# Kernel tuning notes

Hardware: AMD Instinct MI355X
Metric: run time of the kernel (lower is better)

The kernel has to match this reference:

```python
import jax, jax.numpy as jnp
import numpy as np

NH, NUM_H, NUM_W = 8, 4, 4  # num_heads, patch_size


def _grid_sample_zeros(img, grid):
    # img: (N, C, H, W); grid: (N, Ho, Wo, 2) with grid[...,0]=x, grid[...,1]=y in [-1,1]
    # bilinear, align_corners=True, padding_mode='zeros' (each out-of-range tap contributes 0)
    N, C, H, W = img.shape
    gx = (grid[..., 0] + 1.0) * 0.5 * (W - 1)
    gy = (grid[..., 1] + 1.0) * 0.5 * (H - 1)
    x0 = jnp.floor(gx)
    y0 = jnp.floor(gy)
    x1 = x0 + 1.0
    y1 = y0 + 1.0
    wx1 = gx - x0
    wx0 = 1.0 - wx1
    wy1 = gy - y0
    wy0 = 1.0 - wy1

    def per_n(img_n, x0n, x1n, y0n, y1n, w00, w01, w10, w11):
        def tap(xi, yi, w):
            valid = (xi >= 0) & (xi <= W - 1) & (yi >= 0) & (yi <= H - 1)
            xc = jnp.clip(xi, 0, W - 1).astype(jnp.int32)
            yc = jnp.clip(yi, 0, H - 1).astype(jnp.int32)
            return img_n[:, yc, xc] * (w * valid)[None]  # (C, Ho, Wo)
        return tap(x0n, y0n, w00) + tap(x1n, y0n, w01) + tap(x0n, y1n, w10) + tap(x1n, y1n, w11)

    return jax.vmap(per_n)(img, x0, x1, y0, y1, wx0 * wy0, wx1 * wy0, wx0 * wy1, wx1 * wy1)


def _forward(x, global_center, fd_w, fd_b, off_w, off_b, scale_w, scale_b,
             angle_w, angle_b, q_w, q_b, k_w, k_b, v_w, v_b, proj_w, proj_b,
             conv1_w, bn1_g, bn1_b, bn1_m, bn1_v, conv2_w, bn2_g, bn2_b, bn2_m, bn2_v):
    B, C, H, W = x.shape
    K = fd_w.shape[0]
    nh, num_h, num_w = NH, NUM_H, NUM_W
    hd = C // nh
    ws_h, ws_w = H // num_h, W // num_w
    nW = num_h * num_w
    npt = B * nh  # num_predict_total (num_deform = 1)
    S = ws_h * ws_w
    leaky = lambda z: jnp.where(z > 0, z, 0.01 * z)

    # class probabilities: 1x1 conv + softmax over all spatial positions
    logits = jnp.einsum('bchw,kc->bkhw', x, fd_w) + fd_b[None, :, None, None]
    probs = jax.nn.softmax(logits.reshape(B, K, H * W), axis=-1).reshape(B, K, H, W)

    # per-window adaptive-avg-pooled features -> offsets / scales / angles (1x1 convs)
    pooled = leaky(x.reshape(B, C, num_h, ws_h, num_w, ws_w).mean(axis=(3, 5)))  # (B,C,num_h,num_w)

    def head_conv(wt, bi, last):
        o = jnp.einsum('bcij,oc->boij', pooled, wt) + bi[None, :, None, None]
        o = o.transpose(0, 2, 3, 1).reshape(B, num_h, num_w, nh, last)
        return o.transpose(0, 3, 4, 1, 2).reshape(B * nh, last, num_h, num_w)

    off = head_conv(off_w, off_b, 2)
    off = off / jnp.array([H // num_h, W // num_w], jnp.float32)[None, :, None, None]
    scl = head_conv(scale_w, scale_b, 2)
    ang = head_conv(angle_w, angle_b, 1)

    # reference / base coordinates (channel 0 = x/width coord, channel 1 = y/height coord)
    h_lin = jnp.linspace(-1.0, 1.0, H)
    w_lin = jnp.linspace(-1.0, 1.0, W)
    wr_h = h_lin.reshape(num_h, ws_h).mean(axis=1)  # window centers (avg_pool)
    wr_w = w_lin.reshape(num_w, ws_w).mean(axis=1)
    bh = jnp.arange(ws_h, dtype=jnp.float32) * 2.0 / (H - 1)
    bh = bh - bh.mean()
    bw = jnp.arange(ws_w, dtype=jnp.float32) * 2.0 / (W - 1)
    bw = bw - bw.mean()

    # scaled then rotated window coords + offsets; shapes broadcast to (npt,num_h,ws_h,num_w,ws_w)
    wc0 = bw[None, None, None, None, :] * (scl[:, 0, :, None, :, None] + 1.0)
    wc1 = bh[None, None, :, None, None] * (scl[:, 1, :, None, :, None] + 1.0)
    a = ang[:, 0, :, None, :, None]
    sin_a, cos_a = jnp.sin(a), jnp.cos(a)
    r0 = -wc1 * sin_a + wc0 * cos_a
    r1 = wc1 * cos_a + wc0 * sin_a
    c0 = wr_w[None, None, None, :, None] + r0 + off[:, 0, :, None, :, None]
    c1 = wr_h[None, :, None, None, None] + r1 + off[:, 1, :, None, :, None]
    grid = jnp.stack([c0, c1], axis=-1).reshape(npt, H, W, 2)

    # keys over the full map, reshaped so each head-block is sampled by its own grid
    key_feat = jnp.einsum('bhwc,oc->bhwo', x.transpose(0, 2, 3, 1), k_w) + k_b
    key_feat = key_feat.transpose(0, 3, 1, 2).reshape(npt, hd, H, W)
    tx = _grid_sample_zeros(key_feat, grid)
    tx = tx.reshape(npt, hd, num_h, ws_h, num_w, ws_w).transpose(0, 2, 4, 3, 5, 1).reshape(npt * nW, S, hd)

    # probs tiled with torch .repeat semantics (index i -> batch i % B), then sampled
    tp = _grid_sample_zeros(jnp.tile(probs, (nh, 1, 1, 1)), grid)
    tp = tp.reshape(npt, K, num_h, ws_h, num_w, ws_w).transpose(0, 2, 4, 3, 5, 1).reshape(npt * nW, S, K)

    # local class centers; reshape matches torch's raw view (B*nW, nh, K, hd)
    lc = jnp.einsum('nsk,nsd->nkd', tp, tx).reshape(B * nW, nh, K, hd)

    # windowed queries, values from global centers (torch .repeat tiling semantics)
    xw = x.reshape(B, C, num_h, ws_h, num_w, ws_w).transpose(0, 2, 4, 3, 5, 1).reshape(B * nW, S, C)
    q = (xw @ q_w.T + q_b).reshape(B * nW, S, nh, hd).transpose(0, 2, 1, 3)  # (BnW, nh, S, hd)
    gc_rep = jnp.tile(global_center, (nW, 1, 1))
    v = (gc_rep @ v_w.T + v_b).reshape(B * nW, K, nh, hd).transpose(0, 2, 1, 3)  # (BnW, nh, K, hd)

    scale = float(hd) ** -0.5
    dots = jnp.einsum('bnsd,bnkd->bnsk', q, lc) * scale
    attn = jax.nn.softmax(dots, axis=-1)
    out = jnp.einsum('bnsk,bnkd->bnsd', attn, v)  # (BnW, nh, S, hd)

    ctx = out.transpose(0, 2, 1, 3).reshape(B * nW, S, C)
    ctx = (ctx @ proj_w.T + proj_b).transpose(0, 2, 1).reshape(B * nW, C, ws_h, ws_w)
    # patch_recover -> (B, C, H, W)
    ctx = ctx.reshape(B, num_h, num_w, C, ws_h, ws_w).transpose(0, 3, 1, 4, 2, 5).reshape(B, C, H, W)

    def conv_bn_relu(h, wconv, g, bb, m, var):
        h = jax.lax.conv_general_dilated(h, wconv, (1, 1), 'SAME',
                                         dimension_numbers=('NCHW', 'OIHW', 'NCHW'))
        h = (h - m[None, :, None, None]) * jax.lax.rsqrt(var + 1e-5)[None, :, None, None]
        h = h * g[None, :, None, None] + bb[None, :, None, None]
        return jnp.maximum(h, 0.0)

    h1 = jnp.concatenate([x, ctx], axis=1)  # (B, 2C, H, W)
    h1 = conv_bn_relu(h1, conv1_w, bn1_g, bn1_b, bn1_m, bn1_v)
    h1 = conv_bn_relu(h1, conv2_w, bn2_g, bn2_b, bn2_m, bn2_v)  # Dropout2d = identity (eval)
    return h1


def setup_inputs():
    B, C, H, W, K, nh = 2, 512, 128, 128, 32, NH
    ks = jax.random.split(jax.random.key(0), 16)

    def lin(k, o, i, s=1.0):
        return (jax.random.normal(k, (o, i), jnp.float32) * (s / np.sqrt(i))).astype(jnp.float32)

    return {
        'x': jax.random.normal(ks[0], (B, C, H, W), jnp.float32),
        'global_center': jax.random.normal(ks[1], (B, K, C), jnp.float32),
        'fd_w': lin(ks[2], K, C), 'fd_b': jnp.zeros((K,), jnp.float32),
        'off_w': lin(ks[3], nh * 2, C, 4.0), 'off_b': jnp.zeros((nh * 2,), jnp.float32),
        'scale_w': lin(ks[4], nh * 2, C, 4.0), 'scale_b': jnp.zeros((nh * 2,), jnp.float32),
        'angle_w': lin(ks[5], nh, C, 4.0), 'angle_b': jnp.zeros((nh,), jnp.float32),
        'q_w': lin(ks[6], C, C), 'q_b': jnp.zeros((C,), jnp.float32),
        'k_w': lin(ks[7], C, C), 'k_b': jnp.zeros((C,), jnp.float32),
        'v_w': lin(ks[8], C, C), 'v_b': jnp.zeros((C,), jnp.float32),
        'proj_w': lin(ks[9], C, C), 'proj_b': jnp.zeros((C,), jnp.float32),
        'conv1_w': jax.random.normal(ks[10], (C, 2 * C, 3, 3), jnp.float32) / np.sqrt(2 * C * 9.0),
        'bn1_g': jnp.ones((C,), jnp.float32), 'bn1_b': jnp.zeros((C,), jnp.float32),
        'bn1_m': jnp.zeros((C,), jnp.float32), 'bn1_v': jnp.ones((C,), jnp.float32),
        'conv2_w': jax.random.normal(ks[11], (C, C, 3, 3), jnp.float32) / np.sqrt(C * 9.0),
        'bn2_g': jnp.ones((C,), jnp.float32), 'bn2_b': jnp.zeros((C,), jnp.float32),
        'bn2_m': jnp.zeros((C,), jnp.float32), 'bn2_v': jnp.ones((C,), jnp.float32),
    }


def reference(x, global_center, fd_w, fd_b, off_w, off_b, scale_w, scale_b,
              angle_w, angle_b, q_w, q_b, k_w, k_b, v_w, v_b, proj_w, proj_b,
              conv1_w, bn1_g, bn1_b, bn1_m, bn1_v, conv2_w, bn2_g, bn2_b, bn2_m, bn2_v):
    return _forward(x, global_center, fd_w, fd_b, off_w, off_b, scale_w, scale_b,
                    angle_w, angle_b, q_w, q_b, k_w, k_b, v_w, v_b, proj_w, proj_b,
                    conv1_w, bn1_g, bn1_b, bn1_m, bn1_v, conv2_w, bn2_g, bn2_b, bn2_m, bn2_v)
```

## Files before the change

### kernel.cpp

```cpp
#include <hip/hip_runtime.h>
#include <hip/hip_bf16.h>
#include <math.h>

#define HW 16384
#define IMH 128
#define IMW 128

typedef _Float16 f16x8 __attribute__((ext_vector_type(8)));
typedef float f32x4 __attribute__((ext_vector_type(4)));

__device__ __forceinline__ void gload16(const void* g, void* l) {
  __builtin_amdgcn_global_load_lds(
      (const __attribute__((address_space(1))) void*)g,
      (__attribute__((address_space(3))) void*)l, 16, 0, 0);
}

__global__ __launch_bounds__(256) void k_logits(const float* __restrict__ x,
                                                const float* __restrict__ fd_w,
                                                const float* __restrict__ fd_b,
                                                float* __restrict__ probs) {
  __shared__ float w[256 * 32];
  int b = blockIdx.y;
  int pix = blockIdx.x * 256 + threadIdx.x;
  float acc[32];
#pragma unroll
  for (int k = 0; k < 32; k++) acc[k] = fd_b[k];
  const float* xp = x + (size_t)b * 512 * HW + pix;
  for (int half = 0; half < 2; half++) {
    int cbase = half * 256;
    __syncthreads();
    for (int i = threadIdx.x; i < 256 * 32; i += 256) {
      int c = i >> 5, k = i & 31;
      w[i] = fd_w[k * 512 + cbase + c];
    }
    __syncthreads();
    for (int c = 0; c < 256; c++) {
      float xv = xp[(size_t)(cbase + c) * HW];
#pragma unroll
      for (int k = 0; k < 32; k++) acc[k] += xv * w[c * 32 + k];
    }
  }
#pragma unroll
  for (int k = 0; k < 32; k++) probs[((size_t)(b * 32 + k)) * HW + pix] = acc[k];
}

__global__ __launch_bounds__(256) void k_softmax_sp(float* __restrict__ probs) {
  int row = blockIdx.x;
  float* p = probs + (size_t)row * HW;
  __shared__ float red[256];
  float mx = -1e30f;
  for (int i = threadIdx.x; i < HW; i += 256) mx = fmaxf(mx, p[i]);
  red[threadIdx.x] = mx;
  __syncthreads();
  for (int s = 128; s > 0; s >>= 1) {
    if (threadIdx.x < s) red[threadIdx.x] = fmaxf(red[threadIdx.x], red[threadIdx.x + s]);
    __syncthreads();
  }
  mx = red[0];
  __syncthreads();
  float sum = 0.f;
  for (int i = threadIdx.x; i < HW; i += 256) sum += expf(p[i] - mx);
  red[threadIdx.x] = sum;
  __syncthreads();
  for (int s = 128; s > 0; s >>= 1) {
    if (threadIdx.x < s) red[threadIdx.x] += red[threadIdx.x + s];
    __syncthreads();
  }
  float inv = 1.0f / red[0];
  for (int i = threadIdx.x; i < HW; i += 256) p[i] = expf(p[i] - mx) * inv;
}

__global__ __launch_bounds__(256) void k_pool(const float* __restrict__ x,
                                              float* __restrict__ pooled) {
  int b = blockIdx.z, ih = blockIdx.y, iw = blockIdx.x;
  for (int c = threadIdx.x; c < 512; c += 256) {
    const float* xp = x + ((size_t)(b * 512 + c) * IMH + ih * 32) * IMW + iw * 32;
    float s = 0.f;
    for (int r = 0; r < 32; r++)
      for (int cc = 0; cc < 32; cc++) s += xp[r * IMW + cc];
    s *= (1.0f / 1024.0f);
    if (s < 0.f) s *= 0.01f;
    pooled[(b * 512 + c) * 16 + ih * 4 + iw] = s;
  }
}

__global__ __launch_bounds__(256) void k_heads(const float* __restrict__ pooled,
                                               const float* __restrict__ off_w, const float* __restrict__ off_b,
                                               const float* __restrict__ scale_w, const float* __restrict__ scale_b,
                                               const float* __restrict__ angle_w, const float* __restrict__ angle_b,
                                               float* __restrict__ f_off, float* __restrict__ f_scl,
                                               float* __restrict__ f_ang) {
  int b = blockIdx.z, ih = blockIdx.y, iw = blockIdx.x;
  __shared__ float pl[512];
  int ij = ih * 4 + iw;
  for (int c = threadIdx.x; c < 512; c += 256) pl[c] = pooled[(b * 512 + c) * 16 + ij];
  __syncthreads();
  int t = threadIdx.x;
  if (t < 40) {
    const float* wt;
    float bias;
    if (t < 16) { wt = off_w + t * 512; bias = off_b[t]; }
    else if (t < 32) { int u = t - 16; wt = scale_w + u * 512; bias = scale_b[u]; }
    else { int u = t - 32; wt = angle_w + u * 512; bias = angle_b[u]; }
    float s = bias;
    for (int c = 0; c < 512; c++) s += pl[c] * wt[c];
    if (t < 16) {
      int n = t / 2, l = t % 2;
      f_off[((b * 8 + n) * 2 + l) * 16 + ij] = s * (1.0f / 32.0f);
    } else if (t < 32) {
      int u = t - 16;
      int n = u / 2, l = u % 2;
      f_scl[((b * 8 + n) * 2 + l) * 16 + ij] = s;
    } else {
      int n = t - 32;
      f_ang[(b * 8 + n) * 16 + ij] = s;
    }
  }
}

__global__ __launch_bounds__(256) void k_grid(const float* __restrict__ f_off,
                                              const float* __restrict__ f_scl,
                                              const float* __restrict__ f_ang,
                                              float* __restrict__ grid) {
  int p = blockIdx.y;
  int hw = blockIdx.x * 256 + threadIdx.x;
  int h = hw >> 7, w = hw & 127;
  int ih = h >> 5, r = h & 31, iw = w >> 5, cs = w & 31;
  int ij = ih * 4 + iw;
  float off0 = f_off[(p * 2 + 0) * 16 + ij], off1 = f_off[(p * 2 + 1) * 16 + ij];
  float scl0 = f_scl[(p * 2 + 0) * 16 + ij], scl1 = f_scl[(p * 2 + 1) * 16 + ij];
  float a = f_ang[p * 16 + ij];
  float sa = sinf(a), ca = cosf(a);
  float bwv = ((float)cs - 15.5f) * (2.0f / 127.0f);
  float bhv = ((float)r - 15.5f) * (2.0f / 127.0f);
  float wc0 = bwv * (scl0 + 1.0f);
  float wc1 = bhv * (scl1 + 1.0f);
  float wrw = -1.0f + 2.0f * ((float)(iw * 32) + 15.5f) / 127.0f;
  float wrh = -1.0f + 2.0f * ((float)(ih * 32) + 15.5f) / 127.0f;
  float c0 = wrw + (-wc1 * sa + wc0 * ca) + off0;
  float c1 = wrh + (wc1 * ca + wc0 * sa) + off1;
  size_t o = ((size_t)p * HW + hw) * 2;
  grid[o] = c0;
  grid[o + 1] = c1;
}

__global__ __launch_bounds__(256) void k_gsample(const float* __restrict__ img, int CH, int pmod,
                                                 const float* __restrict__ grid,
                                                 float* __restrict__ out) {
  int p = blockIdx.y;
  int hw = blockIdx.x * 256 + threadIdx.x;
  const float* ib = img + (size_t)(p % pmod) * CH * HW;
  float gx = grid[((size_t)p * HW + hw) * 2 + 0];
  float gy = grid[((size_t)p * HW + hw) * 2 + 1];
  gx = (gx + 1.0f) * 0.5f * 127.0f;
  gy = (gy + 1.0f) * 0.5f * 127.0f;
  float x0f = floorf(gx), y0f = floorf(gy);
  float wx1 = gx - x0f, wx0 = 1.0f - wx1;
  float wy1 = gy - y0f, wy0 = 1.0f - wy1;
  int x0 = (int)x0f, y0 = (int)y0f;
  bool vx0 = (x0f >= 0.f) && (x0f <= 127.f);
  bool vx1 = (x0f + 1.0f >= 0.f) && (x0f + 1.0f <= 127.f);
  bool vy0 = (y0f >= 0.f) && (y0f <= 127.f);
  bool vy1 = (y0f + 1.0f >= 0.f) && (y0f + 1.0f <= 127.f);
  int x0c = min(max(x0, 0), 127), x1c = min(max(x0 + 1, 0), 127);
  int y0c = min(max(y0, 0), 127), y1c = min(max(y0 + 1, 0), 127);
  float w00 = wx0 * wy0 * ((vx0 && vy0) ? 1.f : 0.f);
  float w01 = wx1 * wy0 * ((vx1 && vy0) ? 1.f : 0.f);
  float w10 = wx0 * wy1 * ((vx0 && vy1) ? 1.f : 0.f);
  float w11 = wx1 * wy1 * ((vx1 && vy1) ? 1.f : 0.f);
  int o00 = y0c * IMW + x0c, o01 = y0c * IMW + x1c;
  int o10 = y1c * IMW + x0c, o11 = y1c * IMW + x1c;
  for (int c = 0; c < CH; c++) {
    const float* ic = ib + (size_t)c * HW;
    float v = ic[o00] * w00 + ic[o01] * w01 + ic[o10] * w10 + ic[o11] * w11;
    out[((size_t)p * CH + c) * HW + hw] = v;
  }
}

__global__ __launch_bounds__(256) void k_lc(const float* __restrict__ tx,
                                            const float* __restrict__ tp,
                                            float* __restrict__ lc) {
  int idx2 = blockIdx.x;
  int p = idx2 >> 4, win = idx2 & 15;
  int ih = win >> 2, iw = win & 3;
  __shared__ float ltx[64][65];
  __shared__ float ltp[64][33];
  int tid = threadIdx.x;
  int k = tid >> 3, dg = tid & 7;
  float acc[8] = {};
  const float* txp = tx + (size_t)p * 64 * HW;
  const float* tpp = tp + (size_t)p * 32 * HW;
  int base = (ih * 32) * IMW + iw * 32;
  for (int s0 = 0; s0 < 1024; s0 += 64) {
#pragma unroll
    for (int i = 0; i < 16; i++) {
      int linear = tid + i * 256;
      int d = linear >> 6, sl = linear & 63;
      int s = s0 + sl;
      int pix = base + (s >> 5) * IMW + (s & 31);
      ltx[sl][d] = txp[(size_t)d * HW + pix];
    }
#pragma unroll
    for (int i = 0; i < 8; i++) {
      int linear = tid + i * 256;
      int kk = linear >> 6, sl = linear & 63;
      int s = s0 + sl;
      int pix = base + (s >> 5) * IMW + (s & 31);
      ltp[sl][kk] = tpp[(size_t)kk * HW + pix];
    }
    __syncthreads();
    for (int sl = 0; sl < 64; sl++) {
      float tv = ltp[sl][k];
#pragma unroll
      for (int j = 0; j < 8; j++) acc[j] += tv * ltx[sl][dg * 8 + j];
    }
    __syncthreads();
  }
  float* lp = lc + ((size_t)idx2 * 32 + k) * 64 + dg * 8;
#pragma unroll
  for (int j = 0; j < 8; j++) lp[j] = acc[j];
}

__global__ __launch_bounds__(256) void k_v2(const float* __restrict__ gc,
                                            const float* __restrict__ v_w,
                                            const float* __restrict__ v_b,
                                            float* __restrict__ v2) {
  int j = blockIdx.x >> 5, k = blockIdx.x & 31;
  __shared__ float g[512];
  for (int c = threadIdx.x; c < 512; c += 256) g[c] = gc[((size_t)j * 32 + k) * 512 + c];
  __syncthreads();
  for (int o = threadIdx.x; o < 512; o += 256) {
    float s = v_b[o];
    const float* wp = v_w + (size_t)o * 512;
    for (int c = 0; c < 512; c++) s += g[c] * wp[c];
    v2[((size_t)j * 32 + k) * 512 + o] = s;
  }
}

__global__ __launch_bounds__(256) void k_attn(const float* __restrict__ Yq,
                                              const float* __restrict__ lc,
                                              const float* __restrict__ v2,
                                              _Float16* __restrict__ att) {
  int n = blockIdx.x, win = blockIdx.y, b = blockIdx.z;
  int ih = win >> 2, iw = win & 3;
  __shared__ float llc[32 * 64];
  __shared__ float lv[32 * 64];
  int bnw = b * 16 + win;
  const float* lcp = lc + (size_t)(bnw * 8 + n) * 2048;
  const float* vp = v2 + (size_t)(bnw & 1) * 32 * 512 + n * 64;
  for (int i = threadIdx.x; i < 2048; i += 256) {
    llc[i] = lcp[i];
    int k = i >> 6, d = i & 63;
    lv[i] = vp[(size_t)k * 512 + d];
  }
  __syncthreads();
  const float scale = 0.125f;
  for (int rep = 0; rep < 4; rep++) {
    int s = threadIdx.x + rep * 256;
    int w = iw * 32 + (s & 31);
    int pix = (ih * 32 + (s >> 5)) * IMW + w;
    const float* qp = Yq + ((size_t)(b * 512 + n * 64)) * HW + pix;
    float q[64];
#pragma unroll
    for (int d = 0; d < 64; d++) q[d] = qp[(size_t)d * HW];
    float dots[32];
#pragma unroll
    for (int k = 0; k < 32; k++) {
      float s2 = 0.f;
#pragma unroll
      for (int d = 0; d < 64; d++) s2 += q[d] * llc[k * 64 + d];
      dots[k] = s2 * scale;
    }
    float mx = -1e30f;
#pragma unroll
    for (int k = 0; k < 32; k++) mx = fmaxf(mx, dots[k]);
    float sum = 0.f;
#pragma unroll
    for (int k = 0; k < 32; k++) {
      dots[k] = expf(dots[k] - mx);
      sum += dots[k];
    }
    float inv = 1.0f / sum;
    float outv[64];
#pragma unroll
    for (int d = 0; d < 64; d++) outv[d] = 0.f;
#pragma unroll
    for (int k = 0; k < 32; k++) {
      float a = dots[k] * inv;
#pragma unroll
      for (int d = 0; d < 64; d++) outv[d] += a * lv[k * 64 + d];
    }
    int key = (w + 1) & 7;
    _Float16* ob = att + ((size_t)(b * HW) + pix) * 512 + n * 64;
#pragma unroll
    for (int u = 0; u < 8; u++) {
      _Float16 hv[8];
#pragma unroll
      for (int j = 0; j < 8; j++) hv[j] = (_Float16)outv[u * 8 + j];
      *reinterpret_cast<f16x8*>(ob + ((u ^ key) << 3)) = *reinterpret_cast<const f16x8*>(hv);
    }
  }
}

__global__ __launch_bounds__(256) void k_to_hwc(const float* __restrict__ in,
                                                _Float16* __restrict__ out) {
  int h = blockIdx.x, b = blockIdx.y;
  __shared__ _Float16 t[128 * 128];
  for (int cc = 0; cc < 4; cc++) {
    int c0 = cc * 128;
    __syncthreads();
    for (int i = 0; i < 16; i++) {
      int linear = i * 256 + threadIdx.x;
      int c = linear >> 5, w4 = linear & 31;
      float4 v = *reinterpret_cast<const float4*>(
          in + ((size_t)(b * 512 + c0 + c) * IMH + h) * IMW + w4 * 4);
      _Float16* d = t + c * 128 + w4 * 4;
      d[0] = (_Float16)v.x; d[1] = (_Float16)v.y;
      d[2] = (_Float16)v.z; d[3] = (_Float16)v.w;
    }
    __syncthreads();
    for (int i = 0; i < 8; i++) {
      int linear = i * 256 + threadIdx.x;
      int j = linear >> 7, w = linear & 127;
      _Float16 v[8];
#pragma unroll
      for (int u = 0; u < 8; u++) v[u] = t[(j * 8 + u) * 128 + w];
      int c = c0 + j * 8;
      int key = (w + 1) & 7;
      int cs = (c & ~63) | (((((c >> 3) & 7) ^ key) & 7) << 3);
      *reinterpret_cast<f16x8*>(out + (((size_t)(b * IMH + h) * IMW + w) * 512) + cs) =
          *reinterpret_cast<const f16x8*>(v);
    }
  }
}

__global__ __launch_bounds__(256) void k_wxform(const float* __restrict__ w,
                                                _Float16* __restrict__ o_, int Cout, int Cin,
                                                int total) {
  int idx = blockIdx.x * 256 + threadIdx.x;
  if (idx >= total) return;
  int c = idx % Cin;
  int t2 = idx / Cin;
  int oc = t2 % Cout;
  int kk = t2 / Cout;
  int ky = kk / 3, kx = kk % 3;
  float v = w[(((size_t)oc * Cin + c) * 3 + ky) * 3 + kx];
  int key = oc & 7;
  int cs = (c & ~63) | (((((c >> 3) & 7) ^ key) & 7) << 3) | (c & 7);
  o_[((size_t)kk * Cout + oc) * Cin + cs] = (_Float16)v;
}

__global__ __launch_bounds__(256) void k_wxform1x1(const float* __restrict__ w,
                                                   _Float16* __restrict__ o_) {
  int idx = blockIdx.x * 256 + threadIdx.x;
  int c = idx & 511;
  int oc = idx >> 9;
  int key = oc & 7;
  int cs = (c & ~63) | (((((c >> 3) & 7) ^ key) & 7) << 3) | (c & 7);
  o_[((size_t)oc << 9) + cs] = (_Float16)w[idx];
}

__global__ __launch_bounds__(256) void k_gemm_mfma(
    const _Float16* __restrict__ xh, const _Float16* __restrict__ wT,
    const float* __restrict__ bias,
    float* __restrict__ out_f32, _Float16* __restrict__ out_hwc) {
  int mt = blockIdx.x;
  int h = blockIdx.y;
  int b = blockIdx.z;
  __shared__ _Float16 ldsA[128 * 64];
  __shared__ _Float16 ldsB[128 * 64];
  int tid = threadIdx.x;
  int wave = tid >> 6, lane = tid & 63;
  int wr = wave >> 1, wc = wave & 1;
  int l15 = lane & 15, l4 = lane >> 4;
  f32x4 acc[4][4] = {};
  for (int ci = 0; ci < 8; ci++) {
    int c0 = ci << 6;
    for (int it = 0; it < 4; it++) {
      int q = it * 4 + wave;
      gload16(xh + (((size_t)(b * IMH + h) * IMW) + q * 8 + (lane >> 3)) * 512 +
                  c0 + (lane & 7) * 8,
              ldsB + q * 512);
      gload16(wT + ((size_t)(mt * 128 + q * 8 + (lane >> 3))) * 512 + c0 + (lane & 7) * 8,
              ldsA + q * 512);
    }
    __syncthreads();
#pragma unroll
    for (int ks = 0; ks < 2; ks++) {
      f16x8 af[4], bf[4];
#pragma unroll
      for (int m = 0; m < 4; m++) {
        int o = wr * 64 + m * 16 + l15;
        int oct = (ks * 4 + l4) ^ (o & 7);
        af[m] = *reinterpret_cast<const f16x8*>(ldsA + o * 64 + oct * 8);
      }
#pragma unroll
      for (int n = 0; n < 4; n++) {
        int r = wc * 64 + n * 16 + l15;
        int oct = (ks * 4 + l4) ^ ((r + 1) & 7);
        bf[n] = *reinterpret_cast<const f16x8*>(ldsB + r * 64 + oct * 8);
      }
#pragma unroll
      for (int m = 0; m < 4; m++)
#pragma unroll
        for (int n = 0; n < 4; n++)
          acc[m][n] = __builtin_amdgcn_mfma_f32_16x16x32_f16(af[m], bf[n],
                                                             acc[m][n], 0, 0, 0);
    }
    __syncthreads();
  }
#pragma unroll
  for (int m = 0; m < 4; m++) {
#pragma unroll
    for (int n = 0; n < 4; n++) {
      f32x4 v = acc[m][n];
      int px = wc * 64 + n * 16 + l15;
      int obase = mt * 128 + wr * 64 + m * 16 + l4 * 4;
      if (out_hwc) {
        _Float16 hv[4];
#pragma unroll
        for (int r = 0; r < 4; r++) hv[r] = (_Float16)(v[r] + bias[obase + r]);
        int key = (px + 1) & 7;
        int cs = (obase & ~63) | (((((obase >> 3) & 7) ^ key) & 7) << 3) | (obase & 7);
        *reinterpret_cast<uint2*>(out_hwc + ((size_t)(b * IMH + h) * IMW + px) * 512 + cs) =
            *reinterpret_cast<const uint2*>(hv);
      } else {
#pragma unroll
        for (int r = 0; r < 4; r++) {
          int o = obase + r;
          out_f32[((size_t)(b * 512 + o)) * HW + h * IMW + px] = v[r] + bias[o];
        }
      }
    }
  }
}

__global__ __launch_bounds__(256) void k_conv_mfma(
    const _Float16* __restrict__ srcA, const _Float16* __restrict__ srcB,
    int CA, int CB,
    const _Float16* __restrict__ wT,
    const float* __restrict__ bn_g, const float* __restrict__ bn_b,
    const float* __restrict__ bn_m, const float* __restrict__ bn_v,
    float* __restrict__ out_f32, _Float16* __restrict__ out_hwc) {
  int mt = blockIdx.x;
  int h = blockIdx.y;
  int b = blockIdx.z;
  int Cin = CA + CB;
  __shared__ _Float16 ldsA[128 * 64];
  __shared__ _Float16 ldsB[130 * 64];
  int tid = threadIdx.x;
  int wave = tid >> 6, lane = tid & 63;
  int wr = wave >> 1, wc = wave & 1;
  int l15 = lane & 15, l4 = lane >> 4;
  f32x4 acc[4][4] = {};
  if (tid < 32) ((float*)ldsB)[tid] = 0.f;
  else if (tid < 64) ((float*)ldsB)[129 * 32 + (tid - 32)] = 0.f;

  const int nc = Cin >> 6;
  for (int ky = 0; ky < 3; ky++) {
    int hh = h + ky - 1;
    if (hh < 0 || hh > 127) continue;
    for (int ci = 0; ci < nc; ci++) {
      int c0 = ci << 6;
      const _Float16* src;
      int cc0, Cbuf;
      if (c0 < CA) { src = srcA; cc0 = c0; Cbuf = CA; }
      else { src = srcB; cc0 = c0 - CA; Cbuf = CB; }
      for (int it = 0; it < 4; it++) {
        int q = it * 4 + wave;
        gload16(src + (((size_t)(b * IMH + hh) * IMW + q * 8 + (lane >> 3)) * Cbuf +
                       cc0 + (lane & 7) * 8),
                ldsB + 64 + q * 512);
      }
      for (int kx = 0; kx < 3; kx++) {
        const _Float16* wbase =
            wT + ((size_t)((ky * 3 + kx) * 512 + mt * 128)) * Cin + c0;
        for (int it = 0; it < 4; it++) {
          int q = it * 4 + wave;
          gload16(wbase + (size_t)(q * 8 + (lane >> 3)) * Cin + (lane & 7) * 8,
                  ldsA + q * 512);
        }
        __syncthreads();
#pragma unroll
        for (int ks = 0; ks < 2; ks++) {
          f16x8 af[4], bf[4];
#pragma unroll
          for (int m = 0; m < 4; m++) {
            int o = wr * 64 + m * 16 + l15;
            int oct = (ks * 4 + l4) ^ (o & 7);
            af[m] = *reinterpret_cast<const f16x8*>(ldsA + o * 64 + oct * 8);
          }
#pragma unroll
          for (int n = 0; n < 4; n++) {
            int r = wc * 64 + n * 16 + l15 + kx;
            int oct = (ks * 4 + l4) ^ (r & 7);
            bf[n] = *reinterpret_cast<const f16x8*>(ldsB + r * 64 + oct * 8);
          }
#pragma unroll
          for (int m = 0; m < 4; m++)
#pragma unroll
            for (int n = 0; n < 4; n++)
              acc[m][n] = __builtin_amdgcn_mfma_f32_16x16x32_f16(af[m], bf[n],
                                                                 acc[m][n], 0, 0, 0);
        }
        __syncthreads();
      }
    }
  }
#pragma unroll
  for (int m = 0; m < 4; m++) {
#pragma unroll
    for (int n = 0; n < 4; n++) {
      f32x4 v = acc[m][n];
      int px = wc * 64 + n * 16 + l15;
      int obase = mt * 128 + wr * 64 + m * 16 + l4 * 4;
      if (out_hwc) {
        _Float16 hv[4];
#pragma unroll
        for (int r = 0; r < 4; r++) {
          int o = obase + r;
          float sc = bn_g[o] * rsqrtf(bn_v[o] + 1e-5f);
          float sh = bn_b[o] - bn_m[o] * sc;
          hv[r] = (_Float16)fmaxf(v[r] * sc + sh, 0.f);
        }
        int key = (px + 1) & 7;
        int cs = (obase & ~63) | (((((obase >> 3) & 7) ^ key) & 7) << 3) | (obase & 7);
        *reinterpret_cast<uint2*>(out_hwc + ((size_t)(b * IMH + h) * IMW + px) * 512 + cs) =
            *reinterpret_cast<const uint2*>(hv);
      } else {
#pragma unroll
        for (int r = 0; r < 4; r++) {
          int o = obase + r;
          float sc = bn_g[o] * rsqrtf(bn_v[o] + 1e-5f);
          float sh = bn_b[o] - bn_m[o] * sc;
          out_f32[((size_t)(b * 512 + o)) * HW + h * IMW + px] =
              fmaxf(v[r] * sc + sh, 0.f);
        }
      }
    }
  }
}

extern "C" void kernel_launch(void* const* d_in, const int* in_sizes, int n_in,
                              void* d_out, int out_size, void* d_ws, size_t ws_size,
                              hipStream_t stream) {
  const float* x = (const float*)d_in[0];
  const float* gc = (const float*)d_in[1];
  const float* fd_w = (const float*)d_in[2];
  const float* fd_b = (const float*)d_in[3];
  const float* off_w = (const float*)d_in[4];
  const float* off_b = (const float*)d_in[5];
  const float* scale_w = (const float*)d_in[6];
  const float* scale_b = (const float*)d_in[7];
  const float* angle_w = (const float*)d_in[8];
  const float* angle_b = (const float*)d_in[9];
  const float* q_w = (const float*)d_in[10];
  const float* q_b = (const float*)d_in[11];
  const float* k_w = (const float*)d_in[12];
  const float* k_b = (const float*)d_in[13];
  const float* v_w = (const float*)d_in[14];
  const float* v_b = (const float*)d_in[15];
  const float* proj_w = (const float*)d_in[16];
  const float* proj_b = (const float*)d_in[17];
  const float* conv1_w = (const float*)d_in[18];
  const float* bn1_g = (const float*)d_in[19];
  const float* bn1_b = (const float*)d_in[20];
  const float* bn1_m = (const float*)d_in[21];
  const float* bn1_v = (const float*)d_in[22];
  const float* conv2_w = (const float*)d_in[23];
  const float* bn2_g = (const float*)d_in[24];
  const float* bn2_b = (const float*)d_in[25];
  const float* bn2_m = (const float*)d_in[26];
  const float* bn2_v = (const float*)d_in[27];

  float* ws = (float*)d_ws;
  float* f_probs = ws; ws += 1048576;
  float* f_grid = ws; ws += 524288;
  float* f_pooled = ws; ws += 16384;
  float* f_off = ws; ws += 512;
  float* f_scl = ws; ws += 512;
  float* f_ang = ws; ws += 256;
  float* f_lc = ws; ws += 524288;
  float* f_v2 = ws; ws += 32768;
  float* f_tp = ws; ws += 8388608;
  float* f_A = ws; ws += 16777216;
  float* f_B = ws; ws += 16777216;
  float* f_C = ws; ws += 16777216;

  _Float16* xh_early = (_Float16*)f_C;
  _Float16* wTq = (_Float16*)f_lc;
  _Float16* wTk = (_Float16*)(f_lc + 131072);
  _Float16* x_hwc = (_Float16*)f_tp;
  _Float16* h1_hwc = (_Float16*)f_A;
  _Float16* ctx_hwc = (_Float16*)f_B;
  _Float16* wT1 = (_Float16*)(f_B + 8388608);
  _Float16* wT2 = (_Float16*)(f_B + 8388608 + 2359296);
  _Float16* wTp = (_Float16*)(f_B + 8388608 + 2359296 + 1179648);
  _Float16* att_hwc = (_Float16*)d_out;

  k_to_hwc<<<dim3(128, 2), 256, 0, stream>>>(x, xh_early);
  k_wxform1x1<<<dim3(1024), 256, 0, stream>>>(q_w, wTq);
  k_wxform1x1<<<dim3(1024), 256, 0, stream>>>(k_w, wTk);

  k_logits<<<dim3(64, 2), 256, 0, stream>>>(x, fd_w, fd_b, f_probs);
  k_softmax_sp<<<dim3(64), 256, 0, stream>>>(f_probs);
  k_pool<<<dim3(4, 4, 2), 256, 0, stream>>>(x, f_pooled);
  k_heads<<<dim3(4, 4, 2), 256, 0, stream>>>(f_pooled, off_w, off_b, scale_w, scale_b,
                                             angle_w, angle_b, f_off, f_scl, f_ang);
  k_grid<<<dim3(64, 16), 256, 0, stream>>>(f_off, f_scl, f_ang, f_grid);

  k_gemm_mfma<<<dim3(4, 128, 2), 256, 0, stream>>>(xh_early, wTk, k_b, f_A, nullptr);
  k_gemm_mfma<<<dim3(4, 128, 2), 256, 0, stream>>>(xh_early, wTq, q_b, f_B, nullptr);

  k_gsample<<<dim3(64, 16), 256, 0, stream>>>(f_A, 64, 16, f_grid, f_C);
  k_gsample<<<dim3(64, 16), 256, 0, stream>>>(f_probs, 32, 2, f_grid, f_tp);
  k_lc<<<dim3(256), 256, 0, stream>>>(f_C, f_tp, f_lc);
  k_to_hwc<<<dim3(128, 2), 256, 0, stream>>>(x, x_hwc);
  k_v2<<<dim3(64), 256, 0, stream>>>(gc, v_w, v_b, f_v2);
  k_attn<<<dim3(8, 16, 2), 256, 0, stream>>>(f_B, f_lc, f_v2, att_hwc);
  k_wxform1x1<<<dim3(1024), 256, 0, stream>>>(proj_w, wTp);
  k_wxform<<<dim3(18432), 256, 0, stream>>>(conv1_w, wT1, 512, 1024, 9 * 512 * 1024);
  k_wxform<<<dim3(9216), 256, 0, stream>>>(conv2_w, wT2, 512, 512, 9 * 512 * 512);
  k_gemm_mfma<<<dim3(4, 128, 2), 256, 0, stream>>>(att_hwc, wTp, proj_b, nullptr, ctx_hwc);
  k_conv_mfma<<<dim3(4, 128, 2), 256, 0, stream>>>(x_hwc, ctx_hwc, 512, 512, wT1,
                                                   bn1_g, bn1_b, bn1_m, bn1_v,
                                                   nullptr, h1_hwc);
  k_conv_mfma<<<dim3(4, 128, 2), 256, 0, stream>>>(h1_hwc, h1_hwc, 512, 0, wT2,
                                                   bn2_g, bn2_b, bn2_m, bn2_v,
                                                   (float*)d_out, nullptr);
}
```

Baseline: 1.490 ms.

## Fuse grid-sample into windowed lc reduction and keep K/Q in fp16 HWC

```diff
diff --git a/kernel.cpp b/kernel.cpp
--- a/kernel.cpp
+++ b/kernel.cpp
@@ -68,6 +68,20 @@
   }
   float inv = 1.0f / red[0];
   for (int i = threadIdx.x; i < HW; i += 256) p[i] = expf(p[i] - mx) * inv;
+}
+
+__global__ __launch_bounds__(256) void k_probs_t(const float* __restrict__ pr,
+                                                 float* __restrict__ out) {
+  int blk = blockIdx.x, b = blockIdx.y;
+  __shared__ float t[32][257];
+  int tid = threadIdx.x;
+  int px0 = blk * 256;
+  for (int i = 0; i < 32; i++)
+    t[i][tid] = pr[((size_t)(b * 32 + i)) * HW + px0 + tid];
+  __syncthreads();
+  float* op = out + ((size_t)b * HW + px0 + tid) * 32;
+#pragma unroll
+  for (int k = 0; k < 32; k++) op[k] = t[k][tid];
 }
 
 __global__ __launch_bounds__(256) void k_pool(const float* __restrict__ x,
@@ -144,75 +158,87 @@
   grid[o + 1] = c1;
 }
 
-__global__ __launch_bounds__(256) void k_gsample(const float* __restrict__ img, int CH, int pmod,
-                                                 const float* __restrict__ grid,
-                                                 float* __restrict__ out) {
-  int p = blockIdx.y;
-  int hw = blockIdx.x * 256 + threadIdx.x;
-  const float* ib = img + (size_t)(p % pmod) * CH * HW;
-  float gx = grid[((size_t)p * HW + hw) * 2 + 0];
-  float gy = grid[((size_t)p * HW + hw) * 2 + 1];
-  gx = (gx + 1.0f) * 0.5f * 127.0f;
-  gy = (gy + 1.0f) * 0.5f * 127.0f;
-  float x0f = floorf(gx), y0f = floorf(gy);
-  float wx1 = gx - x0f, wx0 = 1.0f - wx1;
-  float wy1 = gy - y0f, wy0 = 1.0f - wy1;
-  int x0 = (int)x0f, y0 = (int)y0f;
-  bool vx0 = (x0f >= 0.f) && (x0f <= 127.f);
-  bool vx1 = (x0f + 1.0f >= 0.f) && (x0f + 1.0f <= 127.f);
-  bool vy0 = (y0f >= 0.f) && (y0f <= 127.f);
-  bool vy1 = (y0f + 1.0f >= 0.f) && (y0f + 1.0f <= 127.f);
-  int x0c = min(max(x0, 0), 127), x1c = min(max(x0 + 1, 0), 127);
-  int y0c = min(max(y0, 0), 127), y1c = min(max(y0 + 1, 0), 127);
-  float w00 = wx0 * wy0 * ((vx0 && vy0) ? 1.f : 0.f);
-  float w01 = wx1 * wy0 * ((vx1 && vy0) ? 1.f : 0.f);
-  float w10 = wx0 * wy1 * ((vx0 && vy1) ? 1.f : 0.f);
-  float w11 = wx1 * wy1 * ((vx1 && vy1) ? 1.f : 0.f);
-  int o00 = y0c * IMW + x0c, o01 = y0c * IMW + x1c;
-  int o10 = y1c * IMW + x0c, o11 = y1c * IMW + x1c;
-  for (int c = 0; c < CH; c++) {
-    const float* ic = ib + (size_t)c * HW;
-    float v = ic[o00] * w00 + ic[o01] * w01 + ic[o10] * w10 + ic[o11] * w11;
-    out[((size_t)p * CH + c) * HW + hw] = v;
-  }
-}
-
-__global__ __launch_bounds__(256) void k_lc(const float* __restrict__ tx,
-                                            const float* __restrict__ tp,
-                                            float* __restrict__ lc) {
+__global__ __launch_bounds__(256) void k_samplc(const _Float16* __restrict__ kf,
+                                                const float* __restrict__ probsT,
+                                                const float* __restrict__ grid,
+                                                float* __restrict__ lc) {
   int idx2 = blockIdx.x;
   int p = idx2 >> 4, win = idx2 & 15;
   int ih = win >> 2, iw = win & 3;
-  __shared__ float ltx[64][65];
-  __shared__ float ltp[64][33];
+  int bk = p >> 3, n = p & 7, bp = p & 1;
+  __shared__ int s_off[128][4];
+  __shared__ float s_w[128][4];
+  __shared__ float s_tx[128][65];
+  __shared__ float s_tp[128][33];
   int tid = threadIdx.x;
   int k = tid >> 3, dg = tid & 7;
   float acc[8] = {};
-  const float* txp = tx + (size_t)p * 64 * HW;
-  const float* tpp = tp + (size_t)p * 32 * HW;
-  int base = (ih * 32) * IMW + iw * 32;
-  for (int s0 = 0; s0 < 1024; s0 += 64) {
-#pragma unroll
-    for (int i = 0; i < 16; i++) {
-      int linear = tid + i * 256;
-      int d = linear >> 6, sl = linear & 63;
-      int s = s0 + sl;
-      int pix = base + (s >> 5) * IMW + (s & 31);
-      ltx[sl][d] = txp[(size_t)d * HW + pix];
-    }
-#pragma unroll
-    for (int i = 0; i < 8; i++) {
-      int linear = tid + i * 256;
-      int kk = linear >> 6, sl = linear & 63;
-      int s = s0 + sl;
-      int pix = base + (s >> 5) * IMW + (s & 31);
-      ltp[sl][kk] = tpp[(size_t)kk * HW + pix];
-    }
-    __syncthreads();
-    for (int sl = 0; sl < 64; sl++) {
-      float tv = ltp[sl][k];
-#pragma unroll
-      for (int j = 0; j < 8; j++) acc[j] += tv * ltx[sl][dg * 8 + j];
+  const _Float16* kfb = kf + (size_t)bk * HW * 512 + n * 64;
+  const float* prb = probsT + (size_t)bp * HW * 32;
+  for (int c0 = 0; c0 < 1024; c0 += 128) {
+    if (tid < 128) {
+      int s = c0 + tid;
+      int pix = (ih * 32 + (s >> 5)) * IMW + iw * 32 + (s & 31);
+      float gx = grid[((size_t)p * HW + pix) * 2 + 0];
+      float gy = grid[((size_t)p * HW + pix) * 2 + 1];
+      gx = (gx + 1.0f) * 0.5f * 127.0f;
+      gy = (gy + 1.0f) * 0.5f * 127.0f;
+      float x0f = floorf(gx), y0f = floorf(gy);
+      float wx1 = gx - x0f, wx0 = 1.0f - wx1;
+      float wy1 = gy - y0f, wy0 = 1.0f - wy1;
+      int x0 = (int)x0f, y0 = (int)y0f;
+      bool vx0 = (x0f >= 0.f) && (x0f <= 127.f);
+      bool vx1 = (x0f + 1.0f >= 0.f) && (x0f + 1.0f <= 127.f);
+      bool vy0 = (y0f >= 0.f) && (y0f <= 127.f);
+      bool vy1 = (y0f + 1.0f >= 0.f) && (y0f + 1.0f <= 127.f);
+      int x0c = min(max(x0, 0), 127), x1c = min(max(x0 + 1, 0), 127);
+      int y0c = min(max(y0, 0), 127), y1c = min(max(y0 + 1, 0), 127);
+      s_off[tid][0] = y0c * IMW + x0c;
+      s_off[tid][1] = y0c * IMW + x1c;
+      s_off[tid][2] = y1c * IMW + x0c;
+      s_off[tid][3] = y1c * IMW + x1c;
+      s_w[tid][0] = wx0 * wy0 * ((vx0 && vy0) ? 1.f : 0.f);
+      s_w[tid][1] = wx1 * wy0 * ((vx1 && vy0) ? 1.f : 0.f);
+      s_w[tid][2] = wx0 * wy1 * ((vx0 && vy1) ? 1.f : 0.f);
+      s_w[tid][3] = wx1 * wy1 * ((vx1 && vy1) ? 1.f : 0.f);
+    }
+    __syncthreads();
+#pragma unroll
+    for (int i = 0; i < 4; i++) {
+      int task = tid + i * 256;
+      int sl = task >> 3, d8 = (task & 7) * 8;
+      float vv[8] = {};
+#pragma unroll
+      for (int t = 0; t < 4; t++) {
+        float wt = s_w[sl][t];
+        f16x8 kv = *reinterpret_cast<const f16x8*>(kfb + (size_t)s_off[sl][t] * 512 + d8);
+#pragma unroll
+        for (int j = 0; j < 8; j++) vv[j] += wt * (float)kv[j];
+      }
+#pragma unroll
+      for (int j = 0; j < 8; j++) s_tx[sl][d8 + j] = vv[j];
+    }
+#pragma unroll
+    for (int i = 0; i < 2; i++) {
+      int task = tid + i * 256;
+      int sl = task >> 2, k8 = (task & 3) * 8;
+      float vv[8] = {};
+#pragma unroll
+      for (int t = 0; t < 4; t++) {
+        float wt = s_w[sl][t];
+        const float* pp = prb + (size_t)s_off[sl][t] * 32 + k8;
+#pragma unroll
+        for (int j = 0; j < 8; j++) vv[j] += wt * pp[j];
+      }
+#pragma unroll
+      for (int j = 0; j < 8; j++) s_tp[sl][k8 + j] = vv[j];
+    }
+    __syncthreads();
+    for (int sl = 0; sl < 128; sl++) {
+      float tv = s_tp[sl][k];
+      const float* xr = &s_tx[sl][dg * 8];
+#pragma unroll
+      for (int j = 0; j < 8; j++) acc[j] += tv * xr[j];
     }
     __syncthreads();
   }
@@ -237,7 +263,7 @@
   }
 }
 
-__global__ __launch_bounds__(256) void k_attn(const float* __restrict__ Yq,
+__global__ __launch_bounds__(256) void k_attn(const _Float16* __restrict__ yq,
                                               const float* __restrict__ lc,
                                               const float* __restrict__ v2,
                                               _Float16* __restrict__ att) {
@@ -259,10 +285,14 @@
     int s = threadIdx.x + rep * 256;
     int w = iw * 32 + (s & 31);
     int pix = (ih * 32 + (s >> 5)) * IMW + w;
-    const float* qp = Yq + ((size_t)(b * 512 + n * 64)) * HW + pix;
+    const _Float16* qp = yq + ((size_t)(b * HW) + pix) * 512 + n * 64;
     float q[64];
 #pragma unroll
-    for (int d = 0; d < 64; d++) q[d] = qp[(size_t)d * HW];
+    for (int u = 0; u < 8; u++) {
+      f16x8 v = *reinterpret_cast<const f16x8*>(qp + u * 8);
+#pragma unroll
+      for (int j = 0; j < 8; j++) q[u * 8 + j] = (float)v[j];
+    }
     float dots[32];
 #pragma unroll
     for (int k = 0; k < 32; k++) {
@@ -363,7 +393,7 @@
 __global__ __launch_bounds__(256) void k_gemm_mfma(
     const _Float16* __restrict__ xh, const _Float16* __restrict__ wT,
     const float* __restrict__ bias,
-    float* __restrict__ out_f32, _Float16* __restrict__ out_hwc) {
+    float* __restrict__ out_f32, _Float16* __restrict__ out_hwc, int swz) {
   int mt = blockIdx.x;
   int h = blockIdx.y;
   int b = blockIdx.z;
@@ -420,7 +450,7 @@
         _Float16 hv[4];
 #pragma unroll
         for (int r = 0; r < 4; r++) hv[r] = (_Float16)(v[r] + bias[obase + r]);
-        int key = (px + 1) & 7;
+        int key = swz ? ((px + 1) & 7) : 0;
         int cs = (obase & ~63) | (((((obase >> 3) & 7) ^ key) & 7) << 3) | (obase & 7);
         *reinterpret_cast<uint2*>(out_hwc + ((size_t)(b * IMH + h) * IMW + px) * 512 + cs) =
             *reinterpret_cast<const uint2*>(hv);
@@ -587,42 +617,43 @@
   float* f_B = ws; ws += 16777216;
   float* f_C = ws; ws += 16777216;
 
-  _Float16* xh_early = (_Float16*)f_C;
   _Float16* wTq = (_Float16*)f_lc;
   _Float16* wTk = (_Float16*)(f_lc + 131072);
-  _Float16* x_hwc = (_Float16*)f_tp;
+  float* probsT = f_tp;
+  _Float16* wT1 = (_Float16*)(f_tp + 1048576);
+  _Float16* wT2 = (_Float16*)(f_tp + 1048576 + 2359296);
+  _Float16* wTp = (_Float16*)(f_tp + 1048576 + 2359296 + 1179648);
+  _Float16* kf_hwc = (_Float16*)f_A;
   _Float16* h1_hwc = (_Float16*)f_A;
-  _Float16* ctx_hwc = (_Float16*)f_B;
-  _Float16* wT1 = (_Float16*)(f_B + 8388608);
-  _Float16* wT2 = (_Float16*)(f_B + 8388608 + 2359296);
-  _Float16* wTp = (_Float16*)(f_B + 8388608 + 2359296 + 1179648);
+  _Float16* yq_hwc = (_Float16*)f_B;
+  _Float16* xh = (_Float16*)f_C;
+  _Float16* ctx_hwc = (_Float16*)(f_C + 8388608);
   _Float16* att_hwc = (_Float16*)d_out;
 
-  k_to_hwc<<<dim3(128, 2), 256, 0, stream>>>(x, xh_early);
   k_wxform1x1<<<dim3(1024), 256, 0, stream>>>(q_w, wTq);
   k_wxform1x1<<<dim3(1024), 256, 0, stream>>>(k_w, wTk);
+  k_wxform1x1<<<dim3(1024), 256, 0, stream>>>(proj_w, wTp);
+  k_wxform<<<dim3(18432), 256, 0, stream>>>(conv1_w, wT1, 512, 1024, 9 * 512 * 1024);
+  k_wxform<<<dim3(9216), 256, 0, stream>>>(conv2_w, wT2, 512, 512, 9 * 512 * 512);
+  k_to_hwc<<<dim3(128, 2), 256, 0, stream>>>(x, xh);
 
   k_logits<<<dim3(64, 2), 256, 0, stream>>>(x, fd_w, fd_b, f_probs);
   k_softmax_sp<<<dim3(64), 256, 0, stream>>>(f_probs);
+  k_probs_t<<<dim3(64, 2), 256, 0, stream>>>(f_probs, probsT);
   k_pool<<<dim3(4, 4, 2), 256, 0, stream>>>(x, f_pooled);
   k_heads<<<dim3(4, 4, 2), 256, 0, stream>>>(f_pooled, off_w, off_b, scale_w, scale_b,
                                              angle_w, angle_b, f_off, f_scl, f_ang);
   k_grid<<<dim3(64, 16), 256, 0, stream>>>(f_off, f_scl, f_ang, f_grid);
 
-  k_gemm_mfma<<<dim3(4, 128, 2), 256, 0, stream>>>(xh_early, wTk, k_b, f_A, nullptr);
-  k_gemm_mfma<<<dim3(4, 128, 2), 256, 0, stream>>>(xh_early, wTq, q_b, f_B, nullptr);
-
-  k_gsample<<<dim3(64, 16), 256, 0, stream>>>(f_A, 64, 16, f_grid, f_C);
-  k_gsample<<<dim3(64, 16), 256, 0, stream>>>(f_probs, 32, 2, f_grid, f_tp);
-  k_lc<<<dim3(256), 256, 0, stream>>>(f_C, f_tp, f_lc);
-  k_to_hwc<<<dim3(128, 2), 256, 0, stream>>>(x, x_hwc);
+  k_gemm_mfma<<<dim3(4, 128, 2), 256, 0, stream>>>(xh, wTk, k_b, nullptr, kf_hwc, 0);
+  k_gemm_mfma<<<dim3(4, 128, 2), 256, 0, stream>>>(xh, wTq, q_b, nullptr, yq_hwc, 0);
+
+  k_samplc<<<dim3(256), 256, 0, stream>>>(kf_hwc, probsT, f_grid, f_lc);
   k_v2<<<dim3(64), 256, 0, stream>>>(gc, v_w, v_b, f_v2);
-  k_attn<<<dim3(8, 16, 2), 256, 0, stream>>>(f_B, f_lc, f_v2, att_hwc);
-  k_wxform1x1<<<dim3(1024), 256, 0, stream>>>(proj_w, wTp);
-  k_wxform<<<dim3(18432), 256, 0, stream>>>(conv1_w, wT1, 512, 1024, 9 * 512 * 1024);
-  k_wxform<<<dim3(9216), 256, 0, stream>>>(conv2_w, wT2, 512, 512, 9 * 512 * 512);
-  k_gemm_mfma<<<dim3(4, 128, 2), 256, 0, stream>>>(att_hwc, wTp, proj_b, nullptr, ctx_hwc);
-  k_conv_mfma<<<dim3(4, 128, 2), 256, 0, stream>>>(x_hwc, ctx_hwc, 512, 512, wT1,
+  k_attn<<<dim3(8, 16, 2), 256, 0, stream>>>(yq_hwc, f_lc, f_v2, att_hwc);
+
+  k_gemm_mfma<<<dim3(4, 128, 2), 256, 0, stream>>>(att_hwc, wTp, proj_b, nullptr, ctx_hwc, 1);
+  k_conv_mfma<<<dim3(4, 128, 2), 256, 0, stream>>>(xh, ctx_hwc, 512, 512, wT1,
                                                    bn1_g, bn1_b, bn1_m, bn1_v,
                                                    nullptr, h1_hwc);
   k_conv_mfma<<<dim3(4, 128, 2), 256, 0, stream>>>(h1_hwc, h1_hwc, 512, 0, wT2,
```

Measured after the change: 1.299 ms. -12.8%, faster.
